# Kernel optimization log

Measured on AMD Instinct MI355X. Metric: run time of the kernel, lower is better.

The kernel has to match this reference:

```python
import jax, jax.numpy as jnp
import numpy as np

DT_RANK = 64
D_STATE = 16


def setup_inputs() -> dict:
    key = jax.random.key(0)
    ks = jax.random.split(key, 6)
    B, L, Di = 2, 2048, 2048
    x = jax.random.normal(ks[0], (B, L, Di), dtype=jnp.float32)
    W_xproj = jax.random.normal(ks[1], (DT_RANK + 2 * D_STATE, Di), dtype=jnp.float32) * (Di ** -0.5)
    W_dt = jax.random.uniform(ks[2], (Di, DT_RANK), dtype=jnp.float32, minval=-(DT_RANK ** -0.5), maxval=DT_RANK ** -0.5)
    dt = jnp.exp(jax.random.uniform(ks[3], (Di,), dtype=jnp.float32) * (np.log(0.1) - np.log(0.001)) + np.log(0.001))
    b_dt = dt + jnp.log(-jnp.expm1(-dt))
    A_log = jnp.log(jnp.broadcast_to(jnp.arange(1, D_STATE + 1, dtype=jnp.float32), (Di, D_STATE)))
    D_param = jnp.ones((Di,), dtype=jnp.float32)
    return {"x": x, "W_xproj": W_xproj, "W_dt": W_dt, "b_dt": b_dt, "A_log": A_log, "D_param": D_param}


def _selective_scan(u, delta, A, Bm, Cm):
    # u, delta: (b, l, d); A: (d, n); Bm, Cm: (b, l, n)
    deltaA = jnp.exp(delta[..., None] * A[None, None])          # (b, l, d, n)
    deltaB_u = delta[..., None] * Bm[:, :, None, :] * u[..., None]  # (b, l, d, n)

    def step(h, inp):
        dA, dBu, c = inp                      # dA,dBu: (b,d,n); c: (b,n)
        h = dA * h + dBu
        y = jnp.einsum('bdn,bn->bd', h, c)
        return h, y

    b, l, d = u.shape
    h0 = jnp.zeros((b, d, A.shape[1]), dtype=u.dtype)
    xs = (jnp.moveaxis(deltaA, 1, 0), jnp.moveaxis(deltaB_u, 1, 0), jnp.moveaxis(Cm, 1, 0))
    _, ys = jax.lax.scan(step, h0, xs)        # ys: (l, b, d)
    return jnp.moveaxis(ys, 0, 1)


def reference(x, W_xproj, W_dt, b_dt, A_log, D_param):
    x_dbl = jnp.einsum('bld,ed->ble', x, W_xproj)  # (b, l, dt_rank + 2*n)
    dlt = x_dbl[..., :DT_RANK]
    Bm = x_dbl[..., DT_RANK:DT_RANK + D_STATE]
    Cm = x_dbl[..., DT_RANK + D_STATE:]
    delta = jax.nn.softplus(jnp.einsum('blr,dr->bld', dlt, W_dt) + b_dt)
    A = -jnp.exp(A_log.astype(jnp.float32))
    y = _selective_scan(x, delta, A, Bm, Cm)
    return y + x * D_param[None, None, :]
```

## Files before the change

### kernel.cpp

```cpp
#include <hip/hip_runtime.h>

#define BATCH 2
#define L_SEQ 2048
#define DI 2048
#define NROW (BATCH * L_SEQ)
#define E_DIM 96
#define RNK 64
#define NST 16
#define NCH 64
#define CL 32
#define SPLITK 16
#define KSL (DI / SPLITK)

#define WS_XDBL 0
#define WS_PART 393216
#define WS_HLOC 393216
#define WS_DSUM (393216 + 4194304)

__device__ __forceinline__ float softplusf(float z) {
    return fmaxf(z, 0.f) + __logf(1.f + __expf(-fabsf(z)));
}

__global__ __launch_bounds__(256) void gemm_xproj_part(const float* __restrict__ x,
                                                       const float* __restrict__ Wx,
                                                       float* __restrict__ part) {
    __shared__ float xs[32][68];
    __shared__ float wsh[32][100];
    const int tid = threadIdx.x;
    const int r0 = blockIdx.x * 64;
    const int kbase0 = blockIdx.y * KSL;
    const int rg = tid >> 4;
    const int cg = tid & 15;

    float acc[4][6];
#pragma unroll
    for (int i = 0; i < 4; i++)
#pragma unroll
        for (int j = 0; j < 6; j++) acc[i][j] = 0.f;

    for (int kt = 0; kt < KSL / 32; kt++) {
        const int kb = kbase0 + kt * 32;
#pragma unroll
        for (int rep = 0; rep < 2; rep++) {
            int i = rep * 256 + tid;
            int row = i >> 3;
            int kq = i & 7;
            float4 v = *(const float4*)&x[(long)(r0 + row) * DI + kb + kq * 4];
            xs[kq * 4 + 0][row] = v.x;
            xs[kq * 4 + 1][row] = v.y;
            xs[kq * 4 + 2][row] = v.z;
            xs[kq * 4 + 3][row] = v.w;
        }
#pragma unroll
        for (int rep = 0; rep < 3; rep++) {
            int i = rep * 256 + tid;
            int e = i >> 3;
            int kq = i & 7;
            float4 v = *(const float4*)&Wx[(long)e * DI + kb + kq * 4];
            wsh[kq * 4 + 0][e] = v.x;
            wsh[kq * 4 + 1][e] = v.y;
            wsh[kq * 4 + 2][e] = v.z;
            wsh[kq * 4 + 3][e] = v.w;
        }
        __syncthreads();
#pragma unroll 8
        for (int k = 0; k < 32; k++) {
            float xr[4], wr[6];
#pragma unroll
            for (int i = 0; i < 4; i++) xr[i] = xs[k][rg * 4 + i];
#pragma unroll
            for (int j = 0; j < 6; j++) wr[j] = wsh[k][cg * 6 + j];
#pragma unroll
            for (int i = 0; i < 4; i++)
#pragma unroll
                for (int j = 0; j < 6; j++) acc[i][j] = fmaf(xr[i], wr[j], acc[i][j]);
        }
        __syncthreads();
    }
    const long sbase = (long)blockIdx.y * NROW * E_DIM;
#pragma unroll
    for (int i = 0; i < 4; i++) {
        long rowb = sbase + (long)(r0 + rg * 4 + i) * E_DIM + cg * 6;
#pragma unroll
        for (int j = 0; j < 6; j++) part[rowb + j] = acc[i][j];
    }
}

__global__ __launch_bounds__(256) void xproj_reduce(const float* __restrict__ part,
                                                    float* __restrict__ xdbl) {
    const int i4 = blockIdx.x * 256 + threadIdx.x;
    const float4* p4 = (const float4*)part;
    float4 s = p4[i4];
#pragma unroll
    for (int sp = 1; sp < SPLITK; sp++) {
        float4 v = p4[(long)sp * (NROW * E_DIM / 4) + i4];
        s.x += v.x; s.y += v.y; s.z += v.z; s.w += v.w;
    }
    ((float4*)xdbl)[i4] = s;
}

__global__ __launch_bounds__(256) void gemm_dt(const float* __restrict__ xdbl,
                                               const float* __restrict__ Wdt,
                                               const float* __restrict__ b_dt,
                                               float* __restrict__ delta) {
    __shared__ float dl[32][68];
    __shared__ float wt[32][132];
    const int tid = threadIdx.x;
    const int row0 = blockIdx.x * 64;
    const int d0 = blockIdx.y * 128;
    const int rg = tid >> 5;
    const int cg = tid & 31;

    float acc[8][4];
#pragma unroll
    for (int i = 0; i < 8; i++)
#pragma unroll
        for (int j = 0; j < 4; j++) acc[i][j] = 0.f;

    for (int kt = 0; kt < 2; kt++) {
        const int kb = kt * 32;
#pragma unroll
        for (int rep = 0; rep < 2; rep++) {
            int i = rep * 256 + tid;
            int row = i >> 3;
            int kq = i & 7;
            float4 v = *(const float4*)&xdbl[(long)(row0 + row) * E_DIM + kb + kq * 4];
            dl[kq * 4 + 0][row] = v.x;
            dl[kq * 4 + 1][row] = v.y;
            dl[kq * 4 + 2][row] = v.z;
            dl[kq * 4 + 3][row] = v.w;
        }
#pragma unroll
        for (int rep = 0; rep < 4; rep++) {
            int i = rep * 256 + tid;
            int col = i >> 3;
            int kq = i & 7;
            float4 v = *(const float4*)&Wdt[(long)(d0 + col) * RNK + kb + kq * 4];
            wt[kq * 4 + 0][col] = v.x;
            wt[kq * 4 + 1][col] = v.y;
            wt[kq * 4 + 2][col] = v.z;
            wt[kq * 4 + 3][col] = v.w;
        }
        __syncthreads();
#pragma unroll 8
        for (int k = 0; k < 32; k++) {
            float xr[8], wr[4];
#pragma unroll
            for (int i = 0; i < 8; i++) xr[i] = dl[k][rg * 8 + i];
#pragma unroll
            for (int j = 0; j < 4; j++) wr[j] = wt[k][cg * 4 + j];
#pragma unroll
            for (int i = 0; i < 8; i++)
#pragma unroll
                for (int j = 0; j < 4; j++) acc[i][j] = fmaf(xr[i], wr[j], acc[i][j]);
        }
        __syncthreads();
    }

    float4 bb = *(const float4*)&b_dt[d0 + cg * 4];
#pragma unroll
    for (int i = 0; i < 8; i++) {
        int row = row0 + rg * 8 + i;
        float4 o;
        o.x = softplusf(acc[i][0] + bb.x);
        o.y = softplusf(acc[i][1] + bb.y);
        o.z = softplusf(acc[i][2] + bb.z);
        o.w = softplusf(acc[i][3] + bb.w);
        *(float4*)&delta[(long)row * DI + d0 + cg * 4] = o;
    }
}

__global__ __launch_bounds__(256) void scan_carry(const float* __restrict__ x,
                                                  const float* __restrict__ delta,
                                                  const float* __restrict__ xdbl,
                                                  const float* __restrict__ A_log,
                                                  float* __restrict__ hloc,
                                                  float* __restrict__ dsumb) {
    __shared__ float bs[CL * NST];
    const int tid = threadIdx.x;
    const int d = blockIdx.x * 256 + tid;
    const int c = blockIdx.y;
    const int b = blockIdx.z;
    const int row0 = b * L_SEQ + c * CL;

    for (int i = tid; i < CL * NST / 4; i += 256) {
        int row = i >> 2, q = i & 3;
        ((float4*)bs)[i] = *(const float4*)&xdbl[(long)(row0 + row) * E_DIM + 64 + q * 4];
    }
    __syncthreads();

    float A[16];
#pragma unroll
    for (int q = 0; q < 4; q++) {
        float4 v = *(const float4*)&A_log[(long)d * NST + q * 4];
        A[q * 4 + 0] = -__expf(v.x);
        A[q * 4 + 1] = -__expf(v.y);
        A[q * 4 + 2] = -__expf(v.z);
        A[q * 4 + 3] = -__expf(v.w);
    }
    float h[16];
#pragma unroll
    for (int n = 0; n < 16; n++) h[n] = 0.f;
    float dsum = 0.f;

    long idx = (long)row0 * DI + d;
    float dn = delta[idx], xn = x[idx];
    for (int ll = 0; ll < CL; ll++) {
        float dc = dn, xc = xn;
        if (ll + 1 < CL) { dn = delta[idx + DI]; xn = x[idx + DI]; }
        float du = dc * xc;
        float bl[16];
#pragma unroll
        for (int q = 0; q < 4; q++) {
            float4 v = *(const float4*)&bs[ll * NST + q * 4];
            bl[q * 4 + 0] = v.x; bl[q * 4 + 1] = v.y; bl[q * 4 + 2] = v.z; bl[q * 4 + 3] = v.w;
        }
#pragma unroll
        for (int n = 0; n < 16; n++)
            h[n] = fmaf(__expf(dc * A[n]), h[n], du * bl[n]);
        dsum += dc;
        idx += DI;
    }

    const long cb = ((long)(b * NCH + c) * DI + d);
#pragma unroll
    for (int q = 0; q < 4; q++)
        *(float4*)&hloc[cb * 16 + q * 4] =
            make_float4(h[q * 4], h[q * 4 + 1], h[q * 4 + 2], h[q * 4 + 3]);
    dsumb[cb] = dsum;
}

__global__ __launch_bounds__(256) void scan_prefix(const float* __restrict__ A_log,
                                                   float* __restrict__ hloc,
                                                   const float* __restrict__ dsumb) {
    const int g = blockIdx.x * 256 + threadIdx.x;
    const int n = g & 15;
    const int d = (g >> 4) & (DI - 1);
    const int b = g >> 15;
    const float An = -__expf(A_log[(long)d * NST + n]);
    float hc = 0.f;
    for (int c = 0; c < NCH; c++) {
        const long cb = ((long)(b * NCH + c) * DI + d);
        float hl = hloc[cb * 16 + n];
        float dsv = dsumb[cb];
        hloc[cb * 16 + n] = hc;
        hc = fmaf(__expf(An * dsv), hc, hl);
    }
}

__global__ __launch_bounds__(256) void scan_out(const float* __restrict__ x,
                                                const float* __restrict__ xdbl,
                                                const float* __restrict__ A_log,
                                                const float* __restrict__ Dp,
                                                const float* __restrict__ hloc,
                                                float* __restrict__ out) {
    __shared__ float bs[CL * NST];
    __shared__ float cs[CL * NST];
    const int tid = threadIdx.x;
    const int d = blockIdx.x * 256 + tid;
    const int c = blockIdx.y;
    const int b = blockIdx.z;
    const int row0 = b * L_SEQ + c * CL;

    for (int i = tid; i < CL * NST / 4; i += 256) {
        int row = i >> 2, q = i & 3;
        ((float4*)bs)[i] = *(const float4*)&xdbl[(long)(row0 + row) * E_DIM + 64 + q * 4];
        ((float4*)cs)[i] = *(const float4*)&xdbl[(long)(row0 + row) * E_DIM + 80 + q * 4];
    }
    __syncthreads();

    float A[16];
#pragma unroll
    for (int q = 0; q < 4; q++) {
        float4 v = *(const float4*)&A_log[(long)d * NST + q * 4];
        A[q * 4 + 0] = -__expf(v.x);
        A[q * 4 + 1] = -__expf(v.y);
        A[q * 4 + 2] = -__expf(v.z);
        A[q * 4 + 3] = -__expf(v.w);
    }
    float h[16];
    const long cb = ((long)(b * NCH + c) * DI + d);
#pragma unroll
    for (int q = 0; q < 4; q++) {
        float4 v = *(const float4*)&hloc[cb * 16 + q * 4];
        h[q * 4 + 0] = v.x; h[q * 4 + 1] = v.y; h[q * 4 + 2] = v.z; h[q * 4 + 3] = v.w;
    }
    const float Dd = Dp[d];

    long idx = (long)row0 * DI + d;
    float dn = out[idx], xn = x[idx];
    for (int ll = 0; ll < CL; ll++) {
        float dc = dn, xc = xn;
        if (ll + 1 < CL) { dn = out[idx + DI]; xn = x[idx + DI]; }
        float du = dc * xc;
        float y = 0.f;
#pragma unroll
        for (int q = 0; q < 4; q++) {
            float4 v = *(const float4*)&bs[ll * NST + q * 4];
            float4 w = *(const float4*)&cs[ll * NST + q * 4];
            float e0 = __expf(dc * A[q * 4 + 0]);
            float e1 = __expf(dc * A[q * 4 + 1]);
            float e2 = __expf(dc * A[q * 4 + 2]);
            float e3 = __expf(dc * A[q * 4 + 3]);
            h[q * 4 + 0] = fmaf(e0, h[q * 4 + 0], du * v.x);
            h[q * 4 + 1] = fmaf(e1, h[q * 4 + 1], du * v.y);
            h[q * 4 + 2] = fmaf(e2, h[q * 4 + 2], du * v.z);
            h[q * 4 + 3] = fmaf(e3, h[q * 4 + 3], du * v.w);
            y = fmaf(h[q * 4 + 0], w.x, y);
            y = fmaf(h[q * 4 + 1], w.y, y);
            y = fmaf(h[q * 4 + 2], w.z, y);
            y = fmaf(h[q * 4 + 3], w.w, y);
        }
        out[idx] = fmaf(xc, Dd, y);
        idx += DI;
    }
}

extern "C" void kernel_launch(void* const* d_in, const int* in_sizes, int n_in,
                              void* d_out, int out_size, void* d_ws, size_t ws_size,
                              hipStream_t stream) {
    const float* x    = (const float*)d_in[0];
    const float* Wx   = (const float*)d_in[1];
    const float* Wdt  = (const float*)d_in[2];
    const float* bdt  = (const float*)d_in[3];
    const float* Alog = (const float*)d_in[4];
    const float* Dp   = (const float*)d_in[5];
    float* out = (float*)d_out;
    float* ws = (float*)d_ws;
    float* xdbl  = ws + WS_XDBL;
    float* partb = ws + WS_PART;
    float* hloc  = ws + WS_HLOC;
    float* dsumb = ws + WS_DSUM;

    gemm_xproj_part<<<dim3(NROW / 64, SPLITK), 256, 0, stream>>>(x, Wx, partb);
    xproj_reduce<<<dim3(NROW * E_DIM / 4 / 256), 256, 0, stream>>>(partb, xdbl);
    gemm_dt<<<dim3(NROW / 64, DI / 128), 256, 0, stream>>>(xdbl, Wdt, bdt, out);
    scan_carry<<<dim3(DI / 256, NCH, BATCH), 256, 0, stream>>>(x, out, xdbl, Alog, hloc, dsumb);
    scan_prefix<<<dim3(BATCH * DI * NST / 256), 256, 0, stream>>>(Alog, hloc, dsumb);
    scan_out<<<dim3(DI / 256, NCH, BATCH), 256, 0, stream>>>(x, xdbl, Alog, Dp, hloc, out);
}
```

Baseline: 201.5 us.

## Halve scan chunk length, double chunk count, deepen load prefetch and unroll

Cuts the scan chunk length from 32 to 16 and doubles the number of chunks, so the carry and output scan kernels launch twice as many blocks with shorter serial loops. The workspace offset for the per-chunk state buffer is doubled to fit the larger hloc array. The delta/x loads are now prefetched two steps ahead, the inner loops are fully unrolled, and the prefix loop is unrolled by 8. In exchange, the serial prefix pass over chunks gets twice as long and the hloc traffic doubles.

```diff
diff --git a/kernel.cpp b/kernel.cpp
--- a/kernel.cpp
+++ b/kernel.cpp
@@ -7,15 +7,15 @@
 #define E_DIM 96
 #define RNK 64
 #define NST 16
-#define NCH 64
-#define CL 32
+#define NCH 128
+#define CL 16
 #define SPLITK 16
 #define KSL (DI / SPLITK)
 
 #define WS_XDBL 0
 #define WS_PART 393216
 #define WS_HLOC 393216
-#define WS_DSUM (393216 + 4194304)
+#define WS_DSUM (393216 + 8388608)
 
 __device__ __forceinline__ float softplusf(float z) {
     return fmaxf(z, 0.f) + __logf(1.f + __expf(-fabsf(z)));
@@ -183,9 +183,9 @@
     const int b = blockIdx.z;
     const int row0 = b * L_SEQ + c * CL;
 
-    for (int i = tid; i < CL * NST / 4; i += 256) {
-        int row = i >> 2, q = i & 3;
-        ((float4*)bs)[i] = *(const float4*)&xdbl[(long)(row0 + row) * E_DIM + 64 + q * 4];
+    if (tid < CL * NST / 4) {
+        int row = tid >> 2, q = tid & 3;
+        ((float4*)bs)[tid] = *(const float4*)&xdbl[(long)(row0 + row) * E_DIM + 64 + q * 4];
     }
     __syncthreads();
 
@@ -204,10 +204,13 @@
     float dsum = 0.f;
 
     long idx = (long)row0 * DI + d;
-    float dn = delta[idx], xn = x[idx];
+    float d0v = delta[idx],      x0v = x[idx];
+    float d1v = delta[idx + DI], x1v = x[idx + DI];
+#pragma unroll
     for (int ll = 0; ll < CL; ll++) {
-        float dc = dn, xc = xn;
-        if (ll + 1 < CL) { dn = delta[idx + DI]; xn = x[idx + DI]; }
+        float dc = d0v, xc = x0v;
+        d0v = d1v; x0v = x1v;
+        if (ll + 2 < CL) { d1v = delta[idx + 2 * DI]; x1v = x[idx + 2 * DI]; }
         float du = dc * xc;
         float bl[16];
 #pragma unroll
@@ -239,6 +242,7 @@
     const int b = g >> 15;
     const float An = -__expf(A_log[(long)d * NST + n]);
     float hc = 0.f;
+#pragma unroll 8
     for (int c = 0; c < NCH; c++) {
         const long cb = ((long)(b * NCH + c) * DI + d);
         float hl = hloc[cb * 16 + n];
@@ -262,10 +266,10 @@
     const int b = blockIdx.z;
     const int row0 = b * L_SEQ + c * CL;
 
-    for (int i = tid; i < CL * NST / 4; i += 256) {
-        int row = i >> 2, q = i & 3;
-        ((float4*)bs)[i] = *(const float4*)&xdbl[(long)(row0 + row) * E_DIM + 64 + q * 4];
-        ((float4*)cs)[i] = *(const float4*)&xdbl[(long)(row0 + row) * E_DIM + 80 + q * 4];
+    if (tid < CL * NST / 4) {
+        int row = tid >> 2, q = tid & 3;
+        ((float4*)bs)[tid] = *(const float4*)&xdbl[(long)(row0 + row) * E_DIM + 64 + q * 4];
+        ((float4*)cs)[tid] = *(const float4*)&xdbl[(long)(row0 + row) * E_DIM + 80 + q * 4];
     }
     __syncthreads();
 
@@ -288,10 +292,13 @@
     const float Dd = Dp[d];
 
     long idx = (long)row0 * DI + d;
-    float dn = out[idx], xn = x[idx];
+    float d0v = out[idx],      x0v = x[idx];
+    float d1v = out[idx + DI], x1v = x[idx + DI];
+#pragma unroll
     for (int ll = 0; ll < CL; ll++) {
-        float dc = dn, xc = xn;
-        if (ll + 1 < CL) { dn = out[idx + DI]; xn = x[idx + DI]; }
+        float dc = d0v, xc = x0v;
+        d0v = d1v; x0v = x1v;
+        if (ll + 2 < CL) { d1v = out[idx + 2 * DI]; x1v = x[idx + 2 * DI]; }
         float du = dc * xc;
         float y = 0.f;
 #pragma unroll
```

Measured after the change: 204.7 us. Within noise of the previous version (+1.6%).
